# Kernel tuning notes

Measured on AMD Instinct MI355X. Metric: run time of the kernel, lower is better.

The kernel has to match this reference:

```python
import jax, jax.numpy as jnp
import numpy as np

D_MODEL, HIDDEN, H, NB = 1024, 128, 16, 32
B, L = 4, 4096


def setup_inputs() -> dict:
    key = jax.random.key(0)
    ks = jax.random.split(key, 6)
    theta_path = jax.random.normal(ks[0], (B, L, H, NB), dtype=jnp.float32)
    content_emb = jax.random.normal(ks[1], (B, L, D_MODEL), dtype=jnp.float32)
    # params (log_Pi init 0.0; final linear weight scaled by 0.01, bias 0, as in torch init)
    log_Pi = jnp.zeros((H, NB), dtype=jnp.float32)
    W1 = jax.random.normal(ks[2], (D_MODEL, HIDDEN), dtype=jnp.float32) / np.sqrt(D_MODEL)
    b1 = jnp.zeros((HIDDEN,), dtype=jnp.float32)
    W2 = (jax.random.normal(ks[3], (HIDDEN, H * NB), dtype=jnp.float32) / np.sqrt(HIDDEN)) * 0.01
    b2 = jnp.zeros((H * NB,), dtype=jnp.float32)
    return {"theta_path": theta_path, "content_emb": content_emb,
            "log_Pi": log_Pi, "W1": W1, "b1": b1, "W2": W2, "b2": b2}


def _affine_combine(c1, c2):
    a1, u1 = c1
    a2, u2 = c2
    return a2 * a1, a2 * u1 + u2


def reference(theta_path, content_emb, log_Pi, W1, b1, W2, b2):
    Bx, Lx, Hx, NBx = theta_path.shape
    # log_R_head: Linear -> GELU(exact) -> Linear, then clamp
    h = jax.nn.gelu(content_emb @ W1 + b1, approximate=False)
    log_R = jnp.clip((h @ W2 + b2).reshape(Bx, Lx, Hx, NBx), -5.0, 5.0)
    R = jnp.exp(log_R)
    # wrapped innovation nu = atan2(sin(-theta), cos(-theta))
    nu = jnp.arctan2(jnp.sin(-theta_path), jnp.cos(-theta_path))
    Pi = jnp.exp(log_Pi)[None, None]            # [1,1,H,NB]
    K = Pi / jnp.maximum(Pi + R, 1e-8)
    alpha = 1.0 - K
    u = K * nu
    # affine recurrence d_t = alpha_t * d_{t-1} + u_t, parallel scan over L
    _, d = jax.lax.associative_scan(_affine_combine, (alpha, u), axis=1)
    return theta_path + d, jnp.broadcast_to(Pi, R.shape), K, R
```

## Files before the change

### kernel.cpp

```cpp
#include <hip/hip_runtime.h>
#include <math.h>

#define B_   4
#define L_   4096
#define C_   512
#define DM_  1024
#define HID_ 128
#define M_   (B_*L_)
#define NC_  128
#define CT_  32

typedef __attribute__((ext_vector_type(8))) short short8;
typedef __attribute__((ext_vector_type(4))) float f32x4;

__device__ __forceinline__ unsigned short f2bf(float f) {
  unsigned u = __float_as_uint(f);
  u += 0x7fffu + ((u >> 16) & 1u);
  return (unsigned short)(u >> 16);
}

__device__ __forceinline__ float wrap_neg(float th) {
  return 6.283185307179586f * rintf(th * 0.15915494309189535f) - th;
}

__global__ __launch_bounds__(256) void k_prep(const float* __restrict__ W1,
                                              const float* __restrict__ W2,
                                              unsigned short* __restrict__ W1T,
                                              unsigned short* __restrict__ W2T) {
  int idx = blockIdx.x * 256 + threadIdx.x;
  if (idx < DM_ * HID_) {
    int n = idx >> 10, k = idx & 1023;
    W1T[idx] = f2bf(W1[(size_t)k * HID_ + n]);
  }
  int i2 = idx - DM_ * HID_;
  if (i2 >= 0 && i2 < HID_ * C_) {
    int n = i2 >> 7, k = i2 & 127;
    W2T[i2] = f2bf(W2[(size_t)k * C_ + n]);
  }
}

__global__ __launch_bounds__(512) void k_mega(const float* __restrict__ X,
                                              const unsigned short* __restrict__ W1T,
                                              const float* __restrict__ b1,
                                              const unsigned short* __restrict__ W2T,
                                              const float* __restrict__ b2,
                                              const float* __restrict__ logPi,
                                              const float* __restrict__ theta,
                                              float* __restrict__ out1,
                                              float* __restrict__ out2,
                                              float* __restrict__ out3,
                                              float* __restrict__ Ab,
                                              float* __restrict__ Ub) {
  __shared__ char lds[49152];
  const int tid  = threadIdx.x;
  const int m0   = blockIdx.x * 64;
  const int lane = tid & 63;
  const int wave = tid >> 6;
  const int wr   = wave >> 2;
  const int wc   = wave & 3;
  const int fr   = lane & 15;
  const int kg   = lane >> 4;

  f32x4 acc[2][2];
#pragma unroll
  for (int i = 0; i < 2; ++i)
#pragma unroll
    for (int j = 0; j < 2; ++j) acc[i][j] = (f32x4){0.f, 0.f, 0.f, 0.f};

  for (int k0 = 0; k0 < DM_; k0 += 64) {
    {
      int row = tid >> 3, k8 = tid & 7;
      const f32x4* src = (const f32x4*)(X + (size_t)(m0 + row) * DM_ + k0 + k8 * 8);
      f32x4 v0 = __builtin_nontemporal_load(src);
      f32x4 v1 = __builtin_nontemporal_load(src + 1);
      uint4 pk;
      pk.x = f2bf(v0[0]) | ((unsigned)f2bf(v0[1]) << 16);
      pk.y = f2bf(v0[2]) | ((unsigned)f2bf(v0[3]) << 16);
      pk.z = f2bf(v1[0]) | ((unsigned)f2bf(v1[1]) << 16);
      pk.w = f2bf(v1[2]) | ((unsigned)f2bf(v1[3]) << 16);
      *(uint4*)(lds + row * 128 + ((k8 ^ (row & 7)) << 4)) = pk;
    }
#pragma unroll
    for (int t = 0; t < 2; ++t) {
      int c = tid + t * 512;
      int n = c >> 3, k8 = c & 7;
      uint4 v = *(const uint4*)(W1T + (size_t)n * DM_ + k0 + k8 * 8);
      *(uint4*)(lds + 8192 + n * 128 + ((k8 ^ (n & 7)) << 4)) = v;
    }
    __syncthreads();
#pragma unroll
    for (int ks = 0; ks < 2; ++ks) {
      short8 a[2], b[2];
#pragma unroll
      for (int i = 0; i < 2; ++i) {
        int row = wr * 32 + i * 16 + fr;
        a[i] = *(const short8*)(lds + row * 128 + (((ks * 4 + kg) ^ (row & 7)) << 4));
      }
#pragma unroll
      for (int j = 0; j < 2; ++j) {
        int col = wc * 32 + j * 16 + fr;
        b[j] = *(const short8*)(lds + 8192 + col * 128 + (((ks * 4 + kg) ^ (col & 7)) << 4));
      }
#pragma unroll
      for (int i = 0; i < 2; ++i)
#pragma unroll
        for (int j = 0; j < 2; ++j)
          acc[i][j] = __builtin_amdgcn_mfma_f32_16x16x32_bf16(a[i], b[j], acc[i][j], 0, 0, 0);
    }
    __syncthreads();
  }
#pragma unroll
  for (int i = 0; i < 2; ++i)
#pragma unroll
    for (int j = 0; j < 2; ++j) {
      int col = wc * 32 + j * 16 + fr;
      float bb = b1[col];
#pragma unroll
      for (int r = 0; r < 4; ++r) {
        int row = wr * 32 + i * 16 + kg * 4 + r;
        float x = acc[i][j][r] + bb;
        float g = 0.5f * x * (1.0f + erff(x * 0.70710678f));
        *(unsigned short*)(lds + 32768 + row * 256 +
                           (((col >> 3) ^ (row & 15)) << 4) + ((col & 7) << 1)) = f2bf(g);
      }
    }

  const int bidx = m0 >> 12;
  const int ch   = ((m0 & 4095) >> 5) + wr;
  const size_t chbase = ((size_t)(bidx * NC_ + ch)) * C_;

  for (int nc = 0; nc < 4; ++nc) {
    const int n0 = nc * 128;
    {
      int n = tid >> 2;
      int k8b = (tid & 3) << 2;
      const unsigned short* src = W2T + (size_t)(n0 + n) * HID_ + k8b * 8;
#pragma unroll
      for (int q = 0; q < 4; ++q) {
        uint4 v = *(const uint4*)(src + q * 8);
        int k8 = k8b + q;
        *(uint4*)(lds + n * 256 + ((k8 ^ (n & 15)) << 4)) = v;
      }
    }
    __syncthreads();

    f32x4 a2[2][2];
#pragma unroll
    for (int i = 0; i < 2; ++i)
#pragma unroll
      for (int j = 0; j < 2; ++j) a2[i][j] = (f32x4){0.f, 0.f, 0.f, 0.f};
#pragma unroll
    for (int ks = 0; ks < 4; ++ks) {
      short8 af[2], bf2[2];
#pragma unroll
      for (int i = 0; i < 2; ++i) {
        int row = wr * 32 + i * 16 + fr;
        af[i] = *(const short8*)(lds + 32768 + row * 256 + (((ks * 4 + kg) ^ (row & 15)) << 4));
      }
#pragma unroll
      for (int j = 0; j < 2; ++j) {
        int col = wc * 32 + j * 16 + fr;
        bf2[j] = *(const short8*)(lds + col * 256 + (((ks * 4 + kg) ^ (col & 15)) << 4));
      }
#pragma unroll
      for (int i = 0; i < 2; ++i)
#pragma unroll
        for (int j = 0; j < 2; ++j)
          a2[i][j] = __builtin_amdgcn_mfma_f32_16x16x32_bf16(af[i], bf2[j], a2[i][j], 0, 0, 0);
    }

#pragma unroll
    for (int j = 0; j < 2; ++j) {
      int col = n0 + wc * 32 + j * 16 + fr;
      float Pi = expf(logPi[col]);
      float bb = b2[col];
      float A16[2], U16[2];
#pragma unroll
      for (int i = 0; i < 2; ++i) {
        float A = 1.f, U = 0.f;
#pragma unroll
        for (int r = 0; r < 4; ++r) {
          int row = m0 + wr * 32 + i * 16 + kg * 4 + r;
          float lr = a2[i][j][r] + bb;
          lr = fminf(5.0f, fmaxf(-5.0f, lr));
          float R = expf(lr);
          float K = Pi / fmaxf(Pi + R, 1e-8f);
          size_t o = (size_t)row * C_ + col;
          __builtin_nontemporal_store(Pi, &out1[o]);
          out2[o] = K;
          __builtin_nontemporal_store(R, &out3[o]);
          float nu = wrap_neg(theta[o]);
          float a = 1.f - K;
          U = a * U + K * nu;
          A = a * A;
        }
        float oA = __shfl_xor(A, 16), oU = __shfl_xor(U, 16);
        if ((kg & 1) == 0) { U = oA * U + oU; A = oA * A; }
        else               { U = A * oU + U;  A = A * oA; }
        oA = __shfl_xor(A, 32); oU = __shfl_xor(U, 32);
        if ((kg & 2) == 0) { U = oA * U + oU; A = oA * A; }
        else               { U = A * oU + U;  A = A * oA; }
        A16[i] = A; U16[i] = U;
      }
      float A32 = A16[1] * A16[0];
      float U32 = A16[1] * U16[0] + U16[1];
      if (kg == j) { Ab[chbase + col] = A32; Ub[chbase + col] = U32; }
    }
    __syncthreads();
  }
}

__global__ __launch_bounds__(256) void k_scan2(const float* __restrict__ Ab,
                                               const float* __restrict__ Ub,
                                               float* __restrict__ D0) {
  __shared__ float cA[16][17], cU[16][17], carry[16][17];
  const int tid = threadIdx.x;
  const int b   = blockIdx.x >> 5;
  const int c0  = (blockIdx.x & 31) * 16;
  const int c_l = tid & 15, s = tid >> 4;
  const int c   = c0 + c_l;
  float A = 1.f, U = 0.f;
#pragma unroll
  for (int k = 0; k < 8; ++k) {
    size_t o = ((size_t)(b * NC_ + s * 8 + k)) * C_ + c;
    float a = Ab[o], u = Ub[o];
    U = a * U + u; A *= a;
  }
  cA[s][c_l] = A; cU[s][c_l] = U;
  __syncthreads();
  if (tid < 16) {
    float P = 0.f;
#pragma unroll
    for (int ss = 0; ss < 16; ++ss) {
      carry[ss][tid] = P;
      P = cA[ss][tid] * P + cU[ss][tid];
    }
  }
  __syncthreads();
  float d = carry[s][c_l];
#pragma unroll
  for (int k = 0; k < 8; ++k) {
    size_t o = ((size_t)(b * NC_ + s * 8 + k)) * C_ + c;
    D0[o] = d;
    d = Ab[o] * d + Ub[o];
  }
}

__global__ __launch_bounds__(256) void k_scan3(const float* __restrict__ Kv,
                                               const float* __restrict__ theta,
                                               const float* __restrict__ D0,
                                               float* __restrict__ out0) {
  const int b  = blockIdx.x / NC_;
  const int ch = blockIdx.x % NC_;
  const int c  = blockIdx.y * 256 + threadIdx.x;
  size_t base = ((size_t)b * L_ + (size_t)ch * CT_) * C_ + c;
  float d = D0[((size_t)(b * NC_ + ch)) * C_ + c];
#pragma unroll 4
  for (int j = 0; j < CT_; ++j) {
    size_t idx = base + (size_t)j * C_;
    float k  = Kv[idx];
    float th = theta[idx];
    float nu = wrap_neg(th);
    d = (1.f - k) * d + k * nu;
    __builtin_nontemporal_store(th + d, &out0[idx]);
  }
}

extern "C" void kernel_launch(void* const* d_in, const int* in_sizes, int n_in,
                              void* d_out, int out_size, void* d_ws, size_t ws_size,
                              hipStream_t stream) {
  const float* theta = (const float*)d_in[0];
  const float* X     = (const float*)d_in[1];
  const float* logPi = (const float*)d_in[2];
  const float* W1    = (const float*)d_in[3];
  const float* b1    = (const float*)d_in[4];
  const float* W2    = (const float*)d_in[5];
  const float* b2    = (const float*)d_in[6];

  float* out = (float*)d_out;
  const size_t S = (size_t)M_ * C_;
  float* out0 = out;
  float* out1 = out + S;
  float* out2 = out + 2 * S;
  float* out3 = out + 3 * S;

  unsigned short* W1T = (unsigned short*)d_ws;
  unsigned short* W2T = W1T + (size_t)DM_ * HID_;
  float* Ab = (float*)(W2T + (size_t)HID_ * C_);
  float* Ub = Ab + (size_t)B_ * NC_ * C_;
  float* D0 = Ub + (size_t)B_ * NC_ * C_;

  hipLaunchKernelGGL(k_prep, dim3(768), dim3(256), 0, stream, W1, W2, W1T, W2T);
  hipLaunchKernelGGL(k_mega, dim3(M_ / 64), dim3(512), 0, stream,
                     X, W1T, b1, W2T, b2, logPi, theta, out1, out2, out3, Ab, Ub);
  hipLaunchKernelGGL(k_scan2, dim3(B_ * 32), dim3(256), 0, stream, Ab, Ub, D0);
  hipLaunchKernelGGL(k_scan3, dim3(B_ * NC_, 2), dim3(256), 0, stream, out2, theta, D0, out0);
}
```

Before: 81.91 us.

## Halve row tile to 32 and double-buffer LDS staging in fused GEMM kernel

The fused GEMM+scan kernel now processes 32 rows per block instead of 64, doubling the grid to 512 blocks for better occupancy across CUs. Both GEMM stages gain double-buffered LDS staging, so the next K-slice (stage 1) or N-chunk (stage 2) is loaded while MFMAs run on the current buffer. This also removes one barrier per iteration. Scan chunk length drops to 16 and the chunk count rises to 256, with k_scan2 adjusted to match. In exchange, each block re-reads all of W1 for half as many rows, which doubles W1 traffic, and the second-level scan does more serial work.

After: 83.25 us. No clear change (+1.6%).

```diff
diff --git a/kernel.cpp b/kernel.cpp
--- a/kernel.cpp
+++ b/kernel.cpp
@@ -7,8 +7,8 @@
 #define DM_  1024
 #define HID_ 128
 #define M_   (B_*L_)
-#define NC_  128
-#define CT_  32
+#define NC_  256
+#define CT_  16
 
 typedef __attribute__((ext_vector_type(8))) short short8;
 typedef __attribute__((ext_vector_type(4))) float f32x4;
@@ -53,7 +53,7 @@
                                               float* __restrict__ Ub) {
   __shared__ char lds[49152];
   const int tid  = threadIdx.x;
-  const int m0   = blockIdx.x * 64;
+  const int m0   = blockIdx.x * 32;
   const int lane = tid & 63;
   const int wave = tid >> 6;
   const int wr   = wave >> 2;
@@ -61,150 +61,128 @@
   const int fr   = lane & 15;
   const int kg   = lane >> 4;
 
-  f32x4 acc[2][2];
-#pragma unroll
-  for (int i = 0; i < 2; ++i)
-#pragma unroll
-    for (int j = 0; j < 2; ++j) acc[i][j] = (f32x4){0.f, 0.f, 0.f, 0.f};
-
-  for (int k0 = 0; k0 < DM_; k0 += 64) {
-    {
-      int row = tid >> 3, k8 = tid & 7;
-      const f32x4* src = (const f32x4*)(X + (size_t)(m0 + row) * DM_ + k0 + k8 * 8);
-      f32x4 v0 = __builtin_nontemporal_load(src);
-      f32x4 v1 = __builtin_nontemporal_load(src + 1);
-      uint4 pk;
-      pk.x = f2bf(v0[0]) | ((unsigned)f2bf(v0[1]) << 16);
-      pk.y = f2bf(v0[2]) | ((unsigned)f2bf(v0[3]) << 16);
-      pk.z = f2bf(v1[0]) | ((unsigned)f2bf(v1[1]) << 16);
-      pk.w = f2bf(v1[2]) | ((unsigned)f2bf(v1[3]) << 16);
-      *(uint4*)(lds + row * 128 + ((k8 ^ (row & 7)) << 4)) = pk;
-    }
-#pragma unroll
-    for (int t = 0; t < 2; ++t) {
-      int c = tid + t * 512;
-      int n = c >> 3, k8 = c & 7;
-      uint4 v = *(const uint4*)(W1T + (size_t)n * DM_ + k0 + k8 * 8);
-      *(uint4*)(lds + 8192 + n * 128 + ((k8 ^ (n & 7)) << 4)) = v;
-    }
-    __syncthreads();
+  f32x4 acc[2];
+  acc[0] = (f32x4){0.f, 0.f, 0.f, 0.f};
+  acc[1] = (f32x4){0.f, 0.f, 0.f, 0.f};
+
+#define STAGE1(bufi, k0)                                                           \
+  {                                                                                \
+    if (tid < 256) {                                                               \
+      int row = tid >> 3, k8 = tid & 7;                                            \
+      const f32x4* src = (const f32x4*)(X + (size_t)(m0 + row) * DM_ + (k0) + k8 * 8); \
+      f32x4 v0 = __builtin_nontemporal_load(src);                                  \
+      f32x4 v1 = __builtin_nontemporal_load(src + 1);                              \
+      uint4 pk;                                                                    \
+      pk.x = f2bf(v0[0]) | ((unsigned)f2bf(v0[1]) << 16);                          \
+      pk.y = f2bf(v0[2]) | ((unsigned)f2bf(v0[3]) << 16);                          \
+      pk.z = f2bf(v1[0]) | ((unsigned)f2bf(v1[1]) << 16);                          \
+      pk.w = f2bf(v1[2]) | ((unsigned)f2bf(v1[3]) << 16);                          \
+      *(uint4*)(lds + (bufi) * 4096 + row * 128 + ((k8 ^ (row & 7)) << 4)) = pk;   \
+    }                                                                              \
+    _Pragma("unroll")                                                              \
+    for (int t = 0; t < 2; ++t) {                                                  \
+      int c = tid + t * 512;                                                       \
+      int n = c >> 3, k8 = c & 7;                                                  \
+      uint4 v = *(const uint4*)(W1T + (size_t)n * DM_ + (k0) + k8 * 8);            \
+      *(uint4*)(lds + 8192 + (bufi) * 16384 + n * 128 + ((k8 ^ (n & 7)) << 4)) = v;\
+    }                                                                              \
+  }
+
+  STAGE1(0, 0);
+  __syncthreads();
+  for (int it = 0; it < 16; ++it) {
+    const int cur = it & 1;
+    if (it < 15) STAGE1(1 - cur, (it + 1) * 64);
 #pragma unroll
     for (int ks = 0; ks < 2; ++ks) {
-      short8 a[2], b[2];
-#pragma unroll
-      for (int i = 0; i < 2; ++i) {
-        int row = wr * 32 + i * 16 + fr;
-        a[i] = *(const short8*)(lds + row * 128 + (((ks * 4 + kg) ^ (row & 7)) << 4));
-      }
+      int row = wr * 16 + fr;
+      short8 a = *(const short8*)(lds + cur * 4096 + row * 128 +
+                                  (((ks * 4 + kg) ^ (row & 7)) << 4));
 #pragma unroll
       for (int j = 0; j < 2; ++j) {
         int col = wc * 32 + j * 16 + fr;
-        b[j] = *(const short8*)(lds + 8192 + col * 128 + (((ks * 4 + kg) ^ (col & 7)) << 4));
+        short8 b = *(const short8*)(lds + 8192 + cur * 16384 + col * 128 +
+                                    (((ks * 4 + kg) ^ (col & 7)) << 4));
+        acc[j] = __builtin_amdgcn_mfma_f32_16x16x32_bf16(a, b, acc[j], 0, 0, 0);
       }
-#pragma unroll
-      for (int i = 0; i < 2; ++i)
-#pragma unroll
-        for (int j = 0; j < 2; ++j)
-          acc[i][j] = __builtin_amdgcn_mfma_f32_16x16x32_bf16(a[i], b[j], acc[i][j], 0, 0, 0);
     }
     __syncthreads();
   }
 #pragma unroll
-  for (int i = 0; i < 2; ++i)
-#pragma unroll
-    for (int j = 0; j < 2; ++j) {
-      int col = wc * 32 + j * 16 + fr;
-      float bb = b1[col];
-#pragma unroll
-      for (int r = 0; r < 4; ++r) {
-        int row = wr * 32 + i * 16 + kg * 4 + r;
-        float x = acc[i][j][r] + bb;
-        float g = 0.5f * x * (1.0f + erff(x * 0.70710678f));
-        *(unsigned short*)(lds + 32768 + row * 256 +
-                           (((col >> 3) ^ (row & 15)) << 4) + ((col & 7) << 1)) = f2bf(g);
-      }
-    }
+  for (int j = 0; j < 2; ++j) {
+    int col = wc * 32 + j * 16 + fr;
+    float bb = b1[col];
+#pragma unroll
+    for (int r = 0; r < 4; ++r) {
+      int row = wr * 16 + kg * 4 + r;
+      float x = acc[j][r] + bb;
+      float g = 0.5f * x * (1.0f + erff(x * 0.70710678f));
+      *(unsigned short*)(lds + 40960 + row * 256 +
+                         (((col >> 3) ^ (row & 15)) << 4) + ((col & 7) << 1)) = f2bf(g);
+    }
+  }
 
   const int bidx = m0 >> 12;
-  const int ch   = ((m0 & 4095) >> 5) + wr;
+  const int ch   = ((m0 & 4095) >> 4) + wr;
   const size_t chbase = ((size_t)(bidx * NC_ + ch)) * C_;
 
-  for (int nc = 0; nc < 4; ++nc) {
-    const int n0 = nc * 128;
+#define STAGE2(bufi, nc)                                                           \
+  {                                                                                \
+    _Pragma("unroll")                                                              \
+    for (int t = 0; t < 2; ++t) {                                                  \
+      int c = tid + t * 512;                                                       \
+      int n = c >> 4, k8 = c & 15;                                                 \
+      uint4 v = *(const uint4*)(W2T + (size_t)((nc) * 64 + n) * HID_ + k8 * 8);    \
+      *(uint4*)(lds + (bufi) * 16384 + n * 256 + ((k8 ^ (n & 15)) << 4)) = v;      \
+    }                                                                              \
+  }
+
+  STAGE2(0, 0);
+  __syncthreads();
+  for (int nc = 0; nc < 8; ++nc) {
+    const int cur = nc & 1;
+    if (nc < 7) STAGE2(1 - cur, nc + 1);
+
+    f32x4 a2 = (f32x4){0.f, 0.f, 0.f, 0.f};
+#pragma unroll
+    for (int ks = 0; ks < 4; ++ks) {
+      int row = wr * 16 + fr;
+      short8 af = *(const short8*)(lds + 40960 + row * 256 +
+                                   (((ks * 4 + kg) ^ (row & 15)) << 4));
+      int col = wc * 16 + fr;
+      short8 bf2 = *(const short8*)(lds + cur * 16384 + col * 256 +
+                                    (((ks * 4 + kg) ^ (col & 15)) << 4));
+      a2 = __builtin_amdgcn_mfma_f32_16x16x32_bf16(af, bf2, a2, 0, 0, 0);
+    }
+
     {
-      int n = tid >> 2;
-      int k8b = (tid & 3) << 2;
-      const unsigned short* src = W2T + (size_t)(n0 + n) * HID_ + k8b * 8;
-#pragma unroll
-      for (int q = 0; q < 4; ++q) {
-        uint4 v = *(const uint4*)(src + q * 8);
-        int k8 = k8b + q;
-        *(uint4*)(lds + n * 256 + ((k8 ^ (n & 15)) << 4)) = v;
-      }
-    }
-    __syncthreads();
-
-    f32x4 a2[2][2];
-#pragma unroll
-    for (int i = 0; i < 2; ++i)
-#pragma unroll
-      for (int j = 0; j < 2; ++j) a2[i][j] = (f32x4){0.f, 0.f, 0.f, 0.f};
-#pragma unroll
-    for (int ks = 0; ks < 4; ++ks) {
-      short8 af[2], bf2[2];
-#pragma unroll
-      for (int i = 0; i < 2; ++i) {
-        int row = wr * 32 + i * 16 + fr;
-        af[i] = *(const short8*)(lds + 32768 + row * 256 + (((ks * 4 + kg) ^ (row & 15)) << 4));
-      }
-#pragma unroll
-      for (int j = 0; j < 2; ++j) {
-        int col = wc * 32 + j * 16 + fr;
-        bf2[j] = *(const short8*)(lds + col * 256 + (((ks * 4 + kg) ^ (col & 15)) << 4));
-      }
-#pragma unroll
-      for (int i = 0; i < 2; ++i)
-#pragma unroll
-        for (int j = 0; j < 2; ++j)
-          a2[i][j] = __builtin_amdgcn_mfma_f32_16x16x32_bf16(af[i], bf2[j], a2[i][j], 0, 0, 0);
-    }
-
-#pragma unroll
-    for (int j = 0; j < 2; ++j) {
-      int col = n0 + wc * 32 + j * 16 + fr;
+      int col = nc * 64 + wc * 16 + fr;
       float Pi = expf(logPi[col]);
       float bb = b2[col];
-      float A16[2], U16[2];
-#pragma unroll
-      for (int i = 0; i < 2; ++i) {
-        float A = 1.f, U = 0.f;
-#pragma unroll
-        for (int r = 0; r < 4; ++r) {
-          int row = m0 + wr * 32 + i * 16 + kg * 4 + r;
-          float lr = a2[i][j][r] + bb;
-          lr = fminf(5.0f, fmaxf(-5.0f, lr));
-          float R = expf(lr);
-          float K = Pi / fmaxf(Pi + R, 1e-8f);
-          size_t o = (size_t)row * C_ + col;
-          __builtin_nontemporal_store(Pi, &out1[o]);
-          out2[o] = K;
-          __builtin_nontemporal_store(R, &out3[o]);
-          float nu = wrap_neg(theta[o]);
-          float a = 1.f - K;
-          U = a * U + K * nu;
-          A = a * A;
-        }
-        float oA = __shfl_xor(A, 16), oU = __shfl_xor(U, 16);
-        if ((kg & 1) == 0) { U = oA * U + oU; A = oA * A; }
-        else               { U = A * oU + U;  A = A * oA; }
-        oA = __shfl_xor(A, 32); oU = __shfl_xor(U, 32);
-        if ((kg & 2) == 0) { U = oA * U + oU; A = oA * A; }
-        else               { U = A * oU + U;  A = A * oA; }
-        A16[i] = A; U16[i] = U;
+      float A = 1.f, U = 0.f;
+#pragma unroll
+      for (int r = 0; r < 4; ++r) {
+        int row = m0 + wr * 16 + kg * 4 + r;
+        float lr = a2[r] + bb;
+        lr = fminf(5.0f, fmaxf(-5.0f, lr));
+        float R = expf(lr);
+        float K = Pi / fmaxf(Pi + R, 1e-8f);
+        size_t o = (size_t)row * C_ + col;
+        __builtin_nontemporal_store(Pi, &out1[o]);
+        out2[o] = K;
+        __builtin_nontemporal_store(R, &out3[o]);
+        float nu = wrap_neg(theta[o]);
+        float a = 1.f - K;
+        U = a * U + K * nu;
+        A = a * A;
       }
-      float A32 = A16[1] * A16[0];
-      float U32 = A16[1] * U16[0] + U16[1];
-      if (kg == j) { Ab[chbase + col] = A32; Ub[chbase + col] = U32; }
+      float oA = __shfl_xor(A, 16), oU = __shfl_xor(U, 16);
+      if ((kg & 1) == 0) { U = oA * U + oU; A = oA * A; }
+      else               { U = A * oU + U;  A = A * oA; }
+      oA = __shfl_xor(A, 32); oU = __shfl_xor(U, 32);
+      if ((kg & 2) == 0) { U = oA * U + oU; A = oA * A; }
+      else               { U = A * oU + U;  A = A * oA; }
+      if (kg == 0) { Ab[chbase + col] = A; Ub[chbase + col] = U; }
     }
     __syncthreads();
   }
@@ -221,8 +199,8 @@
   const int c   = c0 + c_l;
   float A = 1.f, U = 0.f;
 #pragma unroll
-  for (int k = 0; k < 8; ++k) {
-    size_t o = ((size_t)(b * NC_ + s * 8 + k)) * C_ + c;
+  for (int k = 0; k < 16; ++k) {
+    size_t o = ((size_t)(b * NC_ + s * 16 + k)) * C_ + c;
     float a = Ab[o], u = Ub[o];
     U = a * U + u; A *= a;
   }
@@ -239,8 +217,8 @@
   __syncthreads();
   float d = carry[s][c_l];
 #pragma unroll
-  for (int k = 0; k < 8; ++k) {
-    size_t o = ((size_t)(b * NC_ + s * 8 + k)) * C_ + c;
+  for (int k = 0; k < 16; ++k) {
+    size_t o = ((size_t)(b * NC_ + s * 16 + k)) * C_ + c;
     D0[o] = d;
     d = Ab[o] * d + Ub[o];
   }
@@ -291,7 +269,7 @@
   float* D0 = Ub + (size_t)B_ * NC_ * C_;
 
   hipLaunchKernelGGL(k_prep, dim3(768), dim3(256), 0, stream, W1, W2, W1T, W2T);
-  hipLaunchKernelGGL(k_mega, dim3(M_ / 64), dim3(512), 0, stream,
+  hipLaunchKernelGGL(k_mega, dim3(M_ / 32), dim3(512), 0, stream,
                      X, W1T, b1, W2T, b2, logPi, theta, out1, out2, out3, Ab, Ub);
   hipLaunchKernelGGL(k_scan2, dim3(B_ * 32), dim3(256), 0, stream, Ab, Ub, D0);
   hipLaunchKernelGGL(k_scan3, dim3(B_ * NC_, 2), dim3(256), 0, stream, out2, theta, D0, out0);
```
